# Kernel optimization log

Hardware: AMD Instinct MI355X
Metric: run time of the kernel (lower is better)

## Reference

```python
import jax, jax.numpy as jnp
import numpy as np

NUM_HEADS = 16
SIZE_PER_HEAD = 64
HIDDEN = NUM_HEADS * SIZE_PER_HEAD  # 1024
B, F, T = 4, 1024, 1024
NEG_INF = -10000.0


def setup_inputs() -> dict:
    key = jax.random.key(0)
    ks = jax.random.split(key, 6)
    scale = 0.02
    return {
        "from_tensor": jax.random.normal(ks[0], (B, F, HIDDEN), dtype=jnp.float32),
        "to_tensor": jax.random.normal(ks[1], (B, T, HIDDEN), dtype=jnp.float32),
        "attention_mask": jnp.ones((B, F, T), dtype=jnp.float32),
        "Wq": jax.random.normal(ks[2], (HIDDEN, HIDDEN), dtype=jnp.float32) * scale,
        "bq": jnp.zeros((HIDDEN,), dtype=jnp.float32),
        "Wk": jax.random.normal(ks[3], (HIDDEN, HIDDEN), dtype=jnp.float32) * scale,
        "bk": jnp.zeros((HIDDEN,), dtype=jnp.float32),
        "Wv": jax.random.normal(ks[4], (HIDDEN, HIDDEN), dtype=jnp.float32) * scale,
        "bv": jnp.zeros((HIDDEN,), dtype=jnp.float32),
    }


def _split_heads(x, seq_len):
    # [B, S, H*Dh] -> [B, H, S, Dh]
    return x.reshape(B, seq_len, NUM_HEADS, SIZE_PER_HEAD).transpose(0, 2, 1, 3)


def reference(from_tensor, to_tensor, attention_mask, Wq, bq, Wk, bk, Wv, bv):
    # Q/K/V dense projections (query_act/key_act/value_act are None -> linear)
    q = _split_heads(from_tensor @ Wq + bq, F)   # [B,H,F,Dh]
    k = _split_heads(to_tensor @ Wk + bk, T)     # [B,H,T,Dh]
    v = _split_heads(to_tensor @ Wv + bv, T)     # [B,H,T,Dh]

    # scaled dot-product attention scores: [B,H,F,T]
    scores = jnp.einsum("bhfd,bhtd->bhft", q, k) / jnp.sqrt(
        jnp.asarray(SIZE_PER_HEAD, dtype=q.dtype))

    # BERT-style mask adder: mask==1 -> attend, mask==0 -> -10000
    adder = (1.0 - attention_mask[:, None, :, :]) * NEG_INF
    scores = scores + adder

    attention_probs = jax.nn.softmax(scores, axis=-1)  # dropout_prob=0.0

    ctx = jnp.einsum("bhft,bhtd->bhfd", attention_probs, v)  # [B,H,F,Dh]
    ctx = ctx.transpose(0, 2, 1, 3).reshape(B, F, NUM_HEADS * SIZE_PER_HEAD)
    return ctx, attention_probs
```

## Files before the change

kernel.cpp:

```cpp
#include <hip/hip_runtime.h>

typedef unsigned short u16;
typedef __bf16 bf16x8 __attribute__((ext_vector_type(8)));
typedef float f32x4 __attribute__((ext_vector_type(4)));
typedef u16 u16x8 __attribute__((ext_vector_type(8)));

#define NUM_HEADS 16
#define DHEAD 64
#define HIDDEN 1024
#define BATCH 4
#define SEQ 1024

__device__ __forceinline__ u16 f2bf(float x) {
  unsigned u = __float_as_uint(x);
  u = u + 0x7FFFu + ((u >> 16) & 1u);
  return (u16)(u >> 16);
}
__device__ __forceinline__ float bf2f(u16 b) {
  return __uint_as_float(((unsigned)b) << 16);
}

__device__ __forceinline__ void async16(u16* lds, const u16* g) {
  __builtin_amdgcn_global_load_lds(
      (const __attribute__((address_space(1))) void*)g,
      (__attribute__((address_space(3))) void*)lds, 16, 0, 0);
}

__global__ void k_cvt(const float* __restrict__ in, u16* __restrict__ out, int n8) {
  int i = blockIdx.x * 256 + threadIdx.x;
  if (i >= n8) return;
  float4 a = ((const float4*)in)[i * 2];
  float4 b = ((const float4*)in)[i * 2 + 1];
  u16x8 v;
  v[0] = f2bf(a.x); v[1] = f2bf(a.y); v[2] = f2bf(a.z); v[3] = f2bf(a.w);
  v[4] = f2bf(b.x); v[5] = f2bf(b.y); v[6] = f2bf(b.z); v[7] = f2bf(b.w);
  *(u16x8*)&out[(size_t)i * 8] = v;
}

__global__ void k_wtrans(const float* __restrict__ Wq, const float* __restrict__ Wk,
                         const float* __restrict__ Wv, u16* __restrict__ Wt) {
  __shared__ float tile[64][65];
  const float* W = (blockIdx.z == 0) ? Wq : (blockIdx.z == 1) ? Wk : Wv;
  u16* out = Wt + (size_t)blockIdx.z * HIDDEN * HIDDEN;
  int k0 = blockIdx.y * 64, n0 = blockIdx.x * 64;
  int tid = threadIdx.x;
  int r = tid >> 6, c = tid & 63;
#pragma unroll
  for (int i = 0; i < 16; ++i)
    tile[i * 4 + r][c] = W[(size_t)(k0 + i * 4 + r) * HIDDEN + n0 + c];
  __syncthreads();
#pragma unroll
  for (int i = 0; i < 16; ++i)
    out[(size_t)(n0 + i * 4 + r) * HIDDEN + k0 + c] = f2bf(tile[c][i * 4 + r]);
}

__global__ void k_mask(const float* __restrict__ mask, u16* __restrict__ adder,
                       int* __restrict__ flags) {
  int tt = blockIdx.x, ft = blockIdx.y, b = blockIdx.z;
  int tid = threadIdx.x;
  __shared__ int sflag;
  if (tid == 0) sflag = 0;
  __syncthreads();
  int any = 0;
  size_t base = ((size_t)b * SEQ + ft * 128) * SEQ + tt * 128;
  for (int i = 0; i < 64; ++i) {
    int idx = i * 256 + tid;
    int r = idx >> 7, c = idx & 127;
    float v = mask[base + (size_t)r * SEQ + c];
    any |= (v != 1.0f);
    adder[base + (size_t)r * SEQ + c] = f2bf((1.0f - v) * -10000.0f);
  }
  if (any) sflag = 1;
  __syncthreads();
  if (tid == 0) flags[(b * 8 + ft) * 8 + tt] = sflag;
}

__global__ __launch_bounds__(256) void k_gemm(
    const u16* __restrict__ Af, const u16* __restrict__ At,
    const u16* __restrict__ Wt,
    const float* __restrict__ bq, const float* __restrict__ bk, const float* __restrict__ bv,
    u16* __restrict__ Qh, u16* __restrict__ Kh, u16* __restrict__ Vt) {
  __shared__ u16 sA[128 * 64];
  __shared__ u16 sB[128 * 64];
  int which = blockIdx.z;
  const u16* A = (which == 0) ? Af : At;
  const u16* B = Wt + (size_t)which * HIDDEN * HIDDEN;
  const float* bias = (which == 0) ? bq : (which == 1) ? bk : bv;
  int m0 = blockIdx.y * 128, n0 = blockIdx.x * 128;
  int tid = threadIdx.x, w = tid >> 6, lane = tid & 63;
  int wr = w >> 1, wc = w & 1;
  int g = lane >> 4, cc = lane & 15;

  f32x4 acc[4][4] = {};

  int sx[4], srow[4], scol[4];
#pragma unroll
  for (int i = 0; i < 4; ++i) {
    int ch = w * 4 + i;
    int x = ch * 1024 + lane * 16;
    int row = x >> 7;
    int colb = (x & 127) ^ ((row & 7) << 4);
    sx[i] = ch * 512;
    srow[i] = row;
    scol[i] = colb >> 1;
  }

  for (int kt = 0; kt < HIDDEN / 64; ++kt) {
    __syncthreads();
#pragma unroll
    for (int i = 0; i < 4; ++i) {
      async16(&sA[sx[i]], A + (size_t)(m0 + srow[i]) * HIDDEN + kt * 64 + scol[i]);
      async16(&sB[sx[i]], B + (size_t)(n0 + srow[i]) * HIDDEN + kt * 64 + scol[i]);
    }
    asm volatile("s_waitcnt vmcnt(0)" ::: "memory");
    __syncthreads();
#pragma unroll
    for (int kk = 0; kk < 2; ++kk) {
      bf16x8 af[4], bfr[4];
#pragma unroll
      for (int mf = 0; mf < 4; ++mf) {
        int row = wr * 64 + mf * 16 + cc;
        int colb = (kk * 64 + (g << 4)) ^ ((row & 7) << 4);
        af[mf] = *(const bf16x8*)&sA[(row * 128 + colb) >> 1];
      }
#pragma unroll
      for (int nf = 0; nf < 4; ++nf) {
        int row = wc * 64 + nf * 16 + cc;
        int colb = (kk * 64 + (g << 4)) ^ ((row & 7) << 4);
        bfr[nf] = *(const bf16x8*)&sB[(row * 128 + colb) >> 1];
      }
#pragma unroll
      for (int mf = 0; mf < 4; ++mf)
#pragma unroll
        for (int nf = 0; nf < 4; ++nf)
          acc[mf][nf] = __builtin_amdgcn_mfma_f32_16x16x32_bf16(af[mf], bfr[nf], acc[mf][nf], 0, 0, 0);
    }
  }

#pragma unroll
  for (int mf = 0; mf < 4; ++mf) {
#pragma unroll
    for (int nf = 0; nf < 4; ++nf) {
      int n = n0 + wc * 64 + nf * 16 + cc;
      float bval = bias[n];
      int h = n >> 6, d = n & 63;
#pragma unroll
      for (int r = 0; r < 4; ++r) {
        int m = m0 + wr * 64 + mf * 16 + g * 4 + r;
        int b = m >> 10, s = m & 1023;
        u16 o = f2bf(acc[mf][nf][r] + bval);
        if (which == 0)
          Qh[((((size_t)b * NUM_HEADS + h) * SEQ + s) << 6) + d] = o;
        else if (which == 1)
          Kh[((((size_t)b * NUM_HEADS + h) * SEQ + s) << 6) + d] = o;
        else
          Vt[(((size_t)b * NUM_HEADS + h) * 64 + d) * SEQ + s] = o;
      }
    }
  }
}

__global__ __launch_bounds__(256) void k_attn(
    const u16* __restrict__ Qh, const u16* __restrict__ Kh, const u16* __restrict__ Vt,
    const u16* __restrict__ adder, const int* __restrict__ flags,
    float* __restrict__ ctx, float* __restrict__ probs) {
  __shared__ u16 sQ[128 * 64];
  __shared__ u16 sK[128 * 64];
  __shared__ u16 sV[64 * 128];
  __shared__ u16 sP[128 * 128];
  int ft = blockIdx.x, h = blockIdx.y, b = blockIdx.z;
  int f0 = ft * 128;
  int bh = b * NUM_HEADS + h;
  const u16* Qg = Qh + ((size_t)bh * SEQ + f0) * 64;
  const u16* Kg = Kh + (size_t)bh * SEQ * 64;
  const u16* Vg = Vt + (size_t)bh * 64 * SEQ;
  int tid = threadIdx.x, w = tid >> 6, lane = tid & 63;
  int g = lane >> 4, cc = lane & 15;
  const int fbase = w * 32;

  int sx[4], srow7[4], scol7[4], srow8[4], scol8[4];
#pragma unroll
  for (int i = 0; i < 4; ++i) {
    int ch = w * 4 + i;
    int x = ch * 1024 + lane * 16;
    sx[i] = ch * 512;
    int r7 = x >> 7;
    int c7 = (x & 127) ^ ((r7 & 7) << 4);
    srow7[i] = r7; scol7[i] = c7 >> 1;
    int r8 = x >> 8;
    int c8 = (x & 255) ^ ((r8 & 7) << 4);
    srow8[i] = r8; scol8[i] = c8 >> 1;
  }

#pragma unroll
  for (int i = 0; i < 4; ++i)
    async16(&sQ[sx[i]], Qg + (size_t)srow7[i] * 64 + scol7[i]);

  float m_run[8], l_run[8];
#pragma unroll
  for (int i = 0; i < 8; ++i) { m_run[i] = -3.0e38f; l_run[i] = 0.0f; }

  for (int tt = 0; tt < 8; ++tt) {
    __syncthreads();
#pragma unroll
    for (int i = 0; i < 4; ++i)
      async16(&sK[sx[i]], Kg + (size_t)(tt * 128 + srow7[i]) * 64 + scol7[i]);
    asm volatile("s_waitcnt vmcnt(0)" ::: "memory");
    __syncthreads();

    f32x4 s[2][8] = {};
#pragma unroll
    for (int kk = 0; kk < 2; ++kk) {
      bf16x8 aq[2], bk8[8];
#pragma unroll
      for (int mf = 0; mf < 2; ++mf) {
        int row = fbase + mf * 16 + cc;
        int colb = (kk * 64 + (g << 4)) ^ ((row & 7) << 4);
        aq[mf] = *(const bf16x8*)&sQ[(row * 128 + colb) >> 1];
      }
#pragma unroll
      for (int nf = 0; nf < 8; ++nf) {
        int row = nf * 16 + cc;
        int colb = (kk * 64 + (g << 4)) ^ ((row & 7) << 4);
        bk8[nf] = *(const bf16x8*)&sK[(row * 128 + colb) >> 1];
      }
#pragma unroll
      for (int mf = 0; mf < 2; ++mf)
#pragma unroll
        for (int nf = 0; nf < 8; ++nf)
          s[mf][nf] = __builtin_amdgcn_mfma_f32_16x16x32_bf16(aq[mf], bk8[nf], s[mf][nf], 0, 0, 0);
    }
    int flg = flags[(b * 8 + ft) * 8 + tt];
#pragma unroll
    for (int mf = 0; mf < 2; ++mf)
#pragma unroll
      for (int nf = 0; nf < 8; ++nf)
#pragma unroll
        for (int r = 0; r < 4; ++r) s[mf][nf][r] *= 0.125f;
    if (flg) {
      for (int mf = 0; mf < 2; ++mf)
        for (int nf = 0; nf < 8; ++nf)
          for (int r = 0; r < 4; ++r) {
            int frow = f0 + fbase + mf * 16 + g * 4 + r;
            int tcol = tt * 128 + nf * 16 + cc;
            s[mf][nf][r] += bf2f(adder[((size_t)b * SEQ + frow) * SEQ + tcol]);
          }
    }
#pragma unroll
    for (int mf = 0; mf < 2; ++mf)
#pragma unroll
      for (int r = 0; r < 4; ++r) {
        float tmax = s[mf][0][r];
#pragma unroll
        for (int nf = 1; nf < 8; ++nf) tmax = fmaxf(tmax, s[mf][nf][r]);
        tmax = fmaxf(tmax, __shfl_xor(tmax, 1, 16));
        tmax = fmaxf(tmax, __shfl_xor(tmax, 2, 16));
        tmax = fmaxf(tmax, __shfl_xor(tmax, 4, 16));
        tmax = fmaxf(tmax, __shfl_xor(tmax, 8, 16));
        int idx = mf * 4 + r;
        float mnew = fmaxf(m_run[idx], tmax);
        float sum = 0.f;
#pragma unroll
        for (int nf = 0; nf < 8; ++nf) sum += __expf(s[mf][nf][r] - mnew);
        sum += __shfl_xor(sum, 1, 16);
        sum += __shfl_xor(sum, 2, 16);
        sum += __shfl_xor(sum, 4, 16);
        sum += __shfl_xor(sum, 8, 16);
        l_run[idx] = l_run[idx] * __expf(m_run[idx] - mnew) + sum;
        m_run[idx] = mnew;
      }
  }

  float inv_l[8];
#pragma unroll
  for (int i = 0; i < 8; ++i) inv_l[i] = 1.0f / l_run[i];

  f32x4 accO[2][4] = {};

  for (int tt = 0; tt < 8; ++tt) {
    __syncthreads();
#pragma unroll
    for (int i = 0; i < 4; ++i) {
      async16(&sK[sx[i]], Kg + (size_t)(tt * 128 + srow7[i]) * 64 + scol7[i]);
      async16(&sV[sx[i]], Vg + (size_t)srow8[i] * SEQ + tt * 128 + scol8[i]);
    }
    asm volatile("s_waitcnt vmcnt(0)" ::: "memory");
    __syncthreads();

    f32x4 s[2][8] = {};
#pragma unroll
    for (int kk = 0; kk < 2; ++kk) {
      bf16x8 aq[2], bk8[8];
#pragma unroll
      for (int mf = 0; mf < 2; ++mf) {
        int row = fbase + mf * 16 + cc;
        int colb = (kk * 64 + (g << 4)) ^ ((row & 7) << 4);
        aq[mf] = *(const bf16x8*)&sQ[(row * 128 + colb) >> 1];
      }
#pragma unroll
      for (int nf = 0; nf < 8; ++nf) {
        int row = nf * 16 + cc;
        int colb = (kk * 64 + (g << 4)) ^ ((row & 7) << 4);
        bk8[nf] = *(const bf16x8*)&sK[(row * 128 + colb) >> 1];
      }
#pragma unroll
      for (int mf = 0; mf < 2; ++mf)
#pragma unroll
        for (int nf = 0; nf < 8; ++nf)
          s[mf][nf] = __builtin_amdgcn_mfma_f32_16x16x32_bf16(aq[mf], bk8[nf], s[mf][nf], 0, 0, 0);
    }
    int flg = flags[(b * 8 + ft) * 8 + tt];
#pragma unroll
    for (int mf = 0; mf < 2; ++mf)
#pragma unroll
      for (int nf = 0; nf < 8; ++nf)
#pragma unroll
        for (int r = 0; r < 4; ++r) s[mf][nf][r] *= 0.125f;
    if (flg) {
      for (int mf = 0; mf < 2; ++mf)
        for (int nf = 0; nf < 8; ++nf)
          for (int r = 0; r < 4; ++r) {
            int frow = f0 + fbase + mf * 16 + g * 4 + r;
            int tcol = tt * 128 + nf * 16 + cc;
            s[mf][nf][r] += bf2f(adder[((size_t)b * SEQ + frow) * SEQ + tcol]);
          }
    }
#pragma unroll
    for (int mf = 0; mf < 2; ++mf)
#pragma unroll
      for (int nf = 0; nf < 8; ++nf)
#pragma unroll
        for (int r = 0; r < 4; ++r) {
          int idx = mf * 4 + r;
          float p = __expf(s[mf][nf][r] - m_run[idx]) * inv_l[idx];
          int frow = fbase + mf * 16 + g * 4 + r;
          int tcol = nf * 16 + cc;
          probs[(((size_t)bh * SEQ) + f0 + frow) * SEQ + tt * 128 + tcol] = p;
          sP[(frow * 256 + ((tcol * 2) ^ ((frow & 7) << 4))) >> 1] = f2bf(p);
        }
#pragma unroll
    for (int ks = 0; ks < 4; ++ks) {
      bf16x8 ap[2], bv8[4];
#pragma unroll
      for (int mf = 0; mf < 2; ++mf) {
        int row = fbase + mf * 16 + cc;
        int colb = (ks * 64 + (g << 4)) ^ ((row & 7) << 4);
        ap[mf] = *(const bf16x8*)&sP[(row * 256 + colb) >> 1];
      }
#pragma unroll
      for (int nf = 0; nf < 4; ++nf) {
        int row = nf * 16 + cc;
        int colb = (ks * 64 + (g << 4)) ^ ((row & 7) << 4);
        bv8[nf] = *(const bf16x8*)&sV[(row * 256 + colb) >> 1];
      }
#pragma unroll
      for (int mf = 0; mf < 2; ++mf)
#pragma unroll
        for (int nf = 0; nf < 4; ++nf)
          accO[mf][nf] = __builtin_amdgcn_mfma_f32_16x16x32_bf16(ap[mf], bv8[nf], accO[mf][nf], 0, 0, 0);
    }
  }

#pragma unroll
  for (int mf = 0; mf < 2; ++mf)
#pragma unroll
    for (int nf = 0; nf < 4; ++nf)
#pragma unroll
      for (int r = 0; r < 4; ++r) {
        int frow = fbase + mf * 16 + g * 4 + r;
        int d = nf * 16 + cc;
        ctx[((size_t)b * SEQ + f0 + frow) * HIDDEN + h * 64 + d] = accO[mf][nf][r];
      }
}

extern "C" void kernel_launch(void* const* d_in, const int* in_sizes, int n_in,
                              void* d_out, int out_size, void* d_ws, size_t ws_size,
                              hipStream_t stream) {
  const float* from = (const float*)d_in[0];
  const float* to   = (const float*)d_in[1];
  const float* mask = (const float*)d_in[2];
  const float* Wq   = (const float*)d_in[3];
  const float* bq   = (const float*)d_in[4];
  const float* Wk   = (const float*)d_in[5];
  const float* bk   = (const float*)d_in[6];
  const float* Wv   = (const float*)d_in[7];
  const float* bv   = (const float*)d_in[8];

  char* ws = (char*)d_ws;
  u16* Af    = (u16*)(ws);
  u16* At    = (u16*)(ws + 8388608);
  u16* Wt    = (u16*)(ws + 16777216);
  u16* adder = (u16*)(ws + 23068672);
  int* flags = (int*)(ws + 31457280);
  u16* Qh    = (u16*)(ws + 31458304);
  u16* Kh    = (u16*)(ws + 39846912);
  u16* Vt    = (u16*)(ws + 48235520);

  float* ctx = (float*)d_out;
  float* probs = ctx + (size_t)BATCH * SEQ * HIDDEN;

  k_cvt<<<2048, 256, 0, stream>>>(from, Af, 524288);
  k_cvt<<<2048, 256, 0, stream>>>(to, At, 524288);
  k_wtrans<<<dim3(16, 16, 3), 256, 0, stream>>>(Wq, Wk, Wv, Wt);
  k_mask<<<dim3(8, 8, 4), 256, 0, stream>>>(mask, adder, flags);
  k_gemm<<<dim3(8, 32, 3), 256, 0, stream>>>(Af, At, Wt, bq, bk, bv, Qh, Kh, Vt);
  k_attn<<<dim3(8, 16, 4), 256, 0, stream>>>(Qh, Kh, Vt, adder, flags, ctx, probs);
}
```

Before: 211.1 us.

## Double-buffer GEMM and attention K loads, use exp2 softmax, coalesce probs stores

Adds double-buffered LDS prefetch of the next K tile in both the projection GEMM and the two attention passes, so global loads overlap MFMA work. Q fragments are kept in registers instead of LDS, and the mask flags are preloaded into a bitmask. Softmax switches to exp2 with log2e folded into the scale and the mask adder. Probs are now written from the bf16 LDS copy as coalesced vector stores, and the two convert launches are merged into one. The main risk is that probs are stored after bf16 rounding, which loses precision in that output.

```diff
diff --git a/kernel.cpp b/kernel.cpp
--- a/kernel.cpp
+++ b/kernel.cpp
@@ -6,29 +6,37 @@
 typedef u16 u16x8 __attribute__((ext_vector_type(8)));
 
 #define NUM_HEADS 16
-#define DHEAD 64
 #define HIDDEN 1024
 #define BATCH 4
 #define SEQ 1024
-
-__device__ __forceinline__ u16 f2bf(float x) {
+#define C1 0.1803368809109783f
+#define LOG2E 1.4426950408889634f
+
+#define VMCNT0 asm volatile("s_waitcnt vmcnt(0)" ::: "memory")
+#define VMCNT4 asm volatile("s_waitcnt vmcnt(4)" ::: "memory")
+#define BAR __builtin_amdgcn_s_barrier()
+#define SCHED0 __builtin_amdgcn_sched_barrier(0)
+
+static __device__ __forceinline__ u16 f2bf(float x) {
   unsigned u = __float_as_uint(x);
   u = u + 0x7FFFu + ((u >> 16) & 1u);
   return (u16)(u >> 16);
 }
-__device__ __forceinline__ float bf2f(u16 b) {
+static __device__ __forceinline__ float bf2f(u16 b) {
   return __uint_as_float(((unsigned)b) << 16);
 }
-
-__device__ __forceinline__ void async16(u16* lds, const u16* g) {
+static __device__ __forceinline__ void async16(u16* lds, const u16* g) {
   __builtin_amdgcn_global_load_lds(
       (const __attribute__((address_space(1))) void*)g,
       (__attribute__((address_space(3))) void*)lds, 16, 0, 0);
 }
 
-__global__ void k_cvt(const float* __restrict__ in, u16* __restrict__ out, int n8) {
+__global__ void k_cvt(const float* __restrict__ in0, u16* __restrict__ out0,
+                      const float* __restrict__ in1, u16* __restrict__ out1, int n8) {
   int i = blockIdx.x * 256 + threadIdx.x;
   if (i >= n8) return;
+  const float* in = blockIdx.z ? in1 : in0;
+  u16* out = blockIdx.z ? out1 : out0;
   float4 a = ((const float4*)in)[i * 2];
   float4 b = ((const float4*)in)[i * 2 + 1];
   u16x8 v;
@@ -68,7 +76,7 @@
     int r = idx >> 7, c = idx & 127;
     float v = mask[base + (size_t)r * SEQ + c];
     any |= (v != 1.0f);
-    adder[base + (size_t)r * SEQ + c] = f2bf((1.0f - v) * -10000.0f);
+    adder[base + (size_t)r * SEQ + c] = f2bf((1.0f - v) * -10000.0f * LOG2E);
   }
   if (any) sflag = 1;
   __syncthreads();
@@ -80,8 +88,8 @@
     const u16* __restrict__ Wt,
     const float* __restrict__ bq, const float* __restrict__ bk, const float* __restrict__ bv,
     u16* __restrict__ Qh, u16* __restrict__ Kh, u16* __restrict__ Vt) {
-  __shared__ u16 sA[128 * 64];
-  __shared__ u16 sB[128 * 64];
+  __shared__ u16 sA[2][128 * 64];
+  __shared__ u16 sB[2][128 * 64];
   int which = blockIdx.z;
   const u16* A = (which == 0) ? Af : At;
   const u16* B = Wt + (size_t)which * HIDDEN * HIDDEN;
@@ -93,7 +101,9 @@
 
   f32x4 acc[4][4] = {};
 
-  int sx[4], srow[4], scol[4];
+  int sx[4];
+  const u16* aptr[4];
+  const u16* bptr[4];
 #pragma unroll
   for (int i = 0; i < 4; ++i) {
     int ch = w * 4 + i;
@@ -101,19 +111,29 @@
     int row = x >> 7;
     int colb = (x & 127) ^ ((row & 7) << 4);
     sx[i] = ch * 512;
-    srow[i] = row;
-    scol[i] = colb >> 1;
-  }
-
-  for (int kt = 0; kt < HIDDEN / 64; ++kt) {
-    __syncthreads();
-#pragma unroll
-    for (int i = 0; i < 4; ++i) {
-      async16(&sA[sx[i]], A + (size_t)(m0 + srow[i]) * HIDDEN + kt * 64 + scol[i]);
-      async16(&sB[sx[i]], B + (size_t)(n0 + srow[i]) * HIDDEN + kt * 64 + scol[i]);
-    }
-    asm volatile("s_waitcnt vmcnt(0)" ::: "memory");
-    __syncthreads();
+    aptr[i] = A + (size_t)(m0 + row) * HIDDEN + (colb >> 1);
+    bptr[i] = B + (size_t)(n0 + row) * HIDDEN + (colb >> 1);
+  }
+
+#pragma unroll
+  for (int i = 0; i < 4; ++i) {
+    async16(&sA[0][sx[i]], aptr[i]);
+    async16(&sB[0][sx[i]], bptr[i]);
+  }
+
+#pragma unroll 1
+  for (int kt = 0; kt < 16; ++kt) {
+    int cur = kt & 1;
+    VMCNT0;
+    BAR;
+    SCHED0;
+    if (kt < 15) {
+#pragma unroll
+      for (int i = 0; i < 4; ++i) {
+        async16(&sA[cur ^ 1][sx[i]], aptr[i] + (kt + 1) * 64);
+        async16(&sB[cur ^ 1][sx[i]], bptr[i] + (kt + 1) * 64);
+      }
+    }
 #pragma unroll
     for (int kk = 0; kk < 2; ++kk) {
       bf16x8 af[4], bfr[4];
@@ -121,13 +141,13 @@
       for (int mf = 0; mf < 4; ++mf) {
         int row = wr * 64 + mf * 16 + cc;
         int colb = (kk * 64 + (g << 4)) ^ ((row & 7) << 4);
-        af[mf] = *(const bf16x8*)&sA[(row * 128 + colb) >> 1];
+        af[mf] = *(const bf16x8*)&sA[cur][(row * 128 + colb) >> 1];
       }
 #pragma unroll
       for (int nf = 0; nf < 4; ++nf) {
         int row = wc * 64 + nf * 16 + cc;
         int colb = (kk * 64 + (g << 4)) ^ ((row & 7) << 4);
-        bfr[nf] = *(const bf16x8*)&sB[(row * 128 + colb) >> 1];
+        bfr[nf] = *(const bf16x8*)&sB[cur][(row * 128 + colb) >> 1];
       }
 #pragma unroll
       for (int mf = 0; mf < 4; ++mf)
@@ -164,8 +184,7 @@
     const u16* __restrict__ Qh, const u16* __restrict__ Kh, const u16* __restrict__ Vt,
     const u16* __restrict__ adder, const int* __restrict__ flags,
     float* __restrict__ ctx, float* __restrict__ probs) {
-  __shared__ u16 sQ[128 * 64];
-  __shared__ u16 sK[128 * 64];
+  __shared__ u16 sK[2][128 * 64];
   __shared__ u16 sV[64 * 128];
   __shared__ u16 sP[128 * 128];
   int ft = blockIdx.x, h = blockIdx.y, b = blockIdx.z;
@@ -178,7 +197,14 @@
   int g = lane >> 4, cc = lane & 15;
   const int fbase = w * 32;
 
-  int sx[4], srow7[4], scol7[4], srow8[4], scol8[4];
+  int flgmask = 0;
+#pragma unroll
+  for (int tt = 0; tt < 8; ++tt)
+    flgmask |= (flags[(b * 8 + ft) * 8 + tt] != 0) << tt;
+
+  int sx[4];
+  const u16* kbase[4];
+  const u16* vbase[4];
 #pragma unroll
   for (int i = 0; i < 4; ++i) {
     int ch = w * 4 + i;
@@ -186,58 +212,59 @@
     sx[i] = ch * 512;
     int r7 = x >> 7;
     int c7 = (x & 127) ^ ((r7 & 7) << 4);
-    srow7[i] = r7; scol7[i] = c7 >> 1;
+    kbase[i] = Kg + (size_t)r7 * 64 + (c7 >> 1);
     int r8 = x >> 8;
     int c8 = (x & 255) ^ ((r8 & 7) << 4);
-    srow8[i] = r8; scol8[i] = c8 >> 1;
-  }
-
-#pragma unroll
-  for (int i = 0; i < 4; ++i)
-    async16(&sQ[sx[i]], Qg + (size_t)srow7[i] * 64 + scol7[i]);
+    vbase[i] = Vg + (size_t)r8 * SEQ + (c8 >> 1);
+  }
+
+  bf16x8 aq[2][2];
+#pragma unroll
+  for (int kk = 0; kk < 2; ++kk)
+#pragma unroll
+    for (int mf = 0; mf < 2; ++mf)
+      aq[kk][mf] = *(const bf16x8*)&Qg[(size_t)(fbase + mf * 16 + cc) * 64 + kk * 32 + g * 8];
 
   float m_run[8], l_run[8];
 #pragma unroll
   for (int i = 0; i < 8; ++i) { m_run[i] = -3.0e38f; l_run[i] = 0.0f; }
 
+#pragma unroll
+  for (int i = 0; i < 4; ++i) async16(&sK[0][sx[i]], kbase[i]);
+
+#pragma unroll 1
   for (int tt = 0; tt < 8; ++tt) {
-    __syncthreads();
-#pragma unroll
-    for (int i = 0; i < 4; ++i)
-      async16(&sK[sx[i]], Kg + (size_t)(tt * 128 + srow7[i]) * 64 + scol7[i]);
-    asm volatile("s_waitcnt vmcnt(0)" ::: "memory");
-    __syncthreads();
-
+    int cur = tt & 1;
+    VMCNT0;
+    BAR;
+    SCHED0;
+    if (tt < 7) {
+#pragma unroll
+      for (int i = 0; i < 4; ++i)
+        async16(&sK[cur ^ 1][sx[i]], kbase[i] + (tt + 1) * 8192);
+    }
     f32x4 s[2][8] = {};
 #pragma unroll
     for (int kk = 0; kk < 2; ++kk) {
-      bf16x8 aq[2], bk8[8];
-#pragma unroll
-      for (int mf = 0; mf < 2; ++mf) {
-        int row = fbase + mf * 16 + cc;
-        int colb = (kk * 64 + (g << 4)) ^ ((row & 7) << 4);
-        aq[mf] = *(const bf16x8*)&sQ[(row * 128 + colb) >> 1];
-      }
+      bf16x8 bk8[8];
 #pragma unroll
       for (int nf = 0; nf < 8; ++nf) {
         int row = nf * 16 + cc;
         int colb = (kk * 64 + (g << 4)) ^ ((row & 7) << 4);
-        bk8[nf] = *(const bf16x8*)&sK[(row * 128 + colb) >> 1];
+        bk8[nf] = *(const bf16x8*)&sK[cur][(row * 128 + colb) >> 1];
       }
 #pragma unroll
       for (int mf = 0; mf < 2; ++mf)
 #pragma unroll
         for (int nf = 0; nf < 8; ++nf)
-          s[mf][nf] = __builtin_amdgcn_mfma_f32_16x16x32_bf16(aq[mf], bk8[nf], s[mf][nf], 0, 0, 0);
-    }
-    int flg = flags[(b * 8 + ft) * 8 + tt];
+          s[mf][nf] = __builtin_amdgcn_mfma_f32_16x16x32_bf16(aq[kk][mf], bk8[nf], s[mf][nf], 0, 0, 0);
+    }
 #pragma unroll
     for (int mf = 0; mf < 2; ++mf)
 #pragma unroll
       for (int nf = 0; nf < 8; ++nf)
-#pragma unroll
-        for (int r = 0; r < 4; ++r) s[mf][nf][r] *= 0.125f;
-    if (flg) {
+        s[mf][nf] = s[mf][nf] * C1;
+    if ((flgmask >> tt) & 1) {
       for (int mf = 0; mf < 2; ++mf)
         for (int nf = 0; nf < 8; ++nf)
           for (int r = 0; r < 4; ++r) {
@@ -261,12 +288,12 @@
         float mnew = fmaxf(m_run[idx], tmax);
         float sum = 0.f;
 #pragma unroll
-        for (int nf = 0; nf < 8; ++nf) sum += __expf(s[mf][nf][r] - mnew);
+        for (int nf = 0; nf < 8; ++nf) sum += exp2f(s[mf][nf][r] - mnew);
         sum += __shfl_xor(sum, 1, 16);
         sum += __shfl_xor(sum, 2, 16);
         sum += __shfl_xor(sum, 4, 16);
         sum += __shfl_xor(sum, 8, 16);
-        l_run[idx] = l_run[idx] * __expf(m_run[idx] - mnew) + sum;
+        l_run[idx] = l_run[idx] * exp2f(m_run[idx] - mnew) + sum;
         m_run[idx] = mnew;
       }
   }
@@ -277,46 +304,40 @@
 
   f32x4 accO[2][4] = {};
 
+#pragma unroll
+  for (int i = 0; i < 4; ++i) async16(&sK[0][sx[i]], kbase[i]);
+
+#pragma unroll 1
   for (int tt = 0; tt < 8; ++tt) {
-    __syncthreads();
-#pragma unroll
-    for (int i = 0; i < 4; ++i) {
-      async16(&sK[sx[i]], Kg + (size_t)(tt * 128 + srow7[i]) * 64 + scol7[i]);
-      async16(&sV[sx[i]], Vg + (size_t)srow8[i] * SEQ + tt * 128 + scol8[i]);
-    }
-    asm volatile("s_waitcnt vmcnt(0)" ::: "memory");
-    __syncthreads();
+    int cur = tt & 1;
+    VMCNT0;
+    BAR;
+    SCHED0;
+#pragma unroll
+    for (int i = 0; i < 4; ++i) async16(&sV[sx[i]], vbase[i] + tt * 128);
 
     f32x4 s[2][8] = {};
 #pragma unroll
     for (int kk = 0; kk < 2; ++kk) {
-      bf16x8 aq[2], bk8[8];
-#pragma unroll
-      for (int mf = 0; mf < 2; ++mf) {
-        int row = fbase + mf * 16 + cc;
-        int colb = (kk * 64 + (g << 4)) ^ ((row & 7) << 4);
-        aq[mf] = *(const bf16x8*)&sQ[(row * 128 + colb) >> 1];
-      }
+      bf16x8 bk8[8];
 #pragma unroll
       for (int nf = 0; nf < 8; ++nf) {
         int row = nf * 16 + cc;
         int colb = (kk * 64 + (g << 4)) ^ ((row & 7) << 4);
-        bk8[nf] = *(const bf16x8*)&sK[(row * 128 + colb) >> 1];
+        bk8[nf] = *(const bf16x8*)&sK[cur][(row * 128 + colb) >> 1];
       }
 #pragma unroll
       for (int mf = 0; mf < 2; ++mf)
 #pragma unroll
         for (int nf = 0; nf < 8; ++nf)
-          s[mf][nf] = __builtin_amdgcn_mfma_f32_16x16x32_bf16(aq[mf], bk8[nf], s[mf][nf], 0, 0, 0);
-    }
-    int flg = flags[(b * 8 + ft) * 8 + tt];
+          s[mf][nf] = __builtin_amdgcn_mfma_f32_16x16x32_bf16(aq[kk][mf], bk8[nf], s[mf][nf], 0, 0, 0);
+    }
 #pragma unroll
     for (int mf = 0; mf < 2; ++mf)
 #pragma unroll
       for (int nf = 0; nf < 8; ++nf)
-#pragma unroll
-        for (int r = 0; r < 4; ++r) s[mf][nf][r] *= 0.125f;
-    if (flg) {
+        s[mf][nf] = s[mf][nf] * C1;
+    if ((flgmask >> tt) & 1) {
       for (int mf = 0; mf < 2; ++mf)
         for (int nf = 0; nf < 8; ++nf)
           for (int r = 0; r < 4; ++r) {
@@ -332,12 +353,32 @@
 #pragma unroll
         for (int r = 0; r < 4; ++r) {
           int idx = mf * 4 + r;
-          float p = __expf(s[mf][nf][r] - m_run[idx]) * inv_l[idx];
+          float p = exp2f(s[mf][nf][r] - m_run[idx]) * inv_l[idx];
           int frow = fbase + mf * 16 + g * 4 + r;
           int tcol = nf * 16 + cc;
-          probs[(((size_t)bh * SEQ) + f0 + frow) * SEQ + tt * 128 + tcol] = p;
           sP[(frow * 256 + ((tcol * 2) ^ ((frow & 7) << 4))) >> 1] = f2bf(p);
         }
+#pragma unroll
+    for (int sw = 0; sw < 8; ++sw) {
+      int row = fbase + sw * 4 + (lane >> 4);
+      int colb = ((lane & 15) * 16) ^ ((row & 7) << 4);
+      u16x8 pv = *(const u16x8*)&sP[(row * 256 + colb) >> 1];
+      float* dst = &probs[((size_t)bh * SEQ + f0 + row) * SEQ + tt * 128 + (lane & 15) * 8];
+      f32x4 o0 = {bf2f(pv[0]), bf2f(pv[1]), bf2f(pv[2]), bf2f(pv[3])};
+      f32x4 o1 = {bf2f(pv[4]), bf2f(pv[5]), bf2f(pv[6]), bf2f(pv[7])};
+      *(f32x4*)dst = o0;
+      *(f32x4*)(dst + 4) = o1;
+    }
+    if (tt < 7) {
+#pragma unroll
+      for (int i = 0; i < 4; ++i)
+        async16(&sK[cur ^ 1][sx[i]], kbase[i] + (tt + 1) * 8192);
+      VMCNT4;
+    } else {
+      VMCNT0;
+    }
+    BAR;
+    SCHED0;
 #pragma unroll
     for (int ks = 0; ks < 4; ++ks) {
       bf16x8 ap[2], bv8[4];
@@ -399,8 +440,7 @@
   float* ctx = (float*)d_out;
   float* probs = ctx + (size_t)BATCH * SEQ * HIDDEN;
 
-  k_cvt<<<2048, 256, 0, stream>>>(from, Af, 524288);
-  k_cvt<<<2048, 256, 0, stream>>>(to, At, 524288);
+  k_cvt<<<dim3(2048, 1, 2), 256, 0, stream>>>(from, Af, to, At, 524288);
   k_wtrans<<<dim3(16, 16, 3), 256, 0, stream>>>(Wq, Wk, Wv, Wt);
   k_mask<<<dim3(8, 8, 4), 256, 0, stream>>>(mask, adder, flags);
   k_gemm<<<dim3(8, 32, 3), 256, 0, stream>>>(Af, At, Wt, bq, bk, bv, Qh, Kh, Vt);
```

Measured after the change: 234.4 us. +11.0%, slower.

## Fuse convert launches, skip unmasked adder writes, stage V transpose via LDS, use exp2

Applied to the files above, without the earlier changes.

The two input conversion launches are merged into one grid. The mask kernel now first scans the tile with vectorized loads and writes the bf16 adder (pre-scaled by log2e) only when the tile contains masked entries. The V projection epilogue transposes its tile through shared memory so the transposed stores are coalesced 16-byte writes instead of scattered 2-byte ones. Attention folds log2e into the score scale and switches exp to exp2f. Together these aim to cut mask-write traffic, uncoalesced stores and launch overhead, at the cost of extra LDS syncs in the GEMM epilogue and a second mask read when any tile is masked.

```diff
diff --git a/kernel.cpp b/kernel.cpp
--- a/kernel.cpp
+++ b/kernel.cpp
@@ -4,31 +4,37 @@
 typedef __bf16 bf16x8 __attribute__((ext_vector_type(8)));
 typedef float f32x4 __attribute__((ext_vector_type(4)));
 typedef u16 u16x8 __attribute__((ext_vector_type(8)));
+typedef u16 u16x4 __attribute__((ext_vector_type(4)));
 
 #define NUM_HEADS 16
-#define DHEAD 64
 #define HIDDEN 1024
 #define BATCH 4
 #define SEQ 1024
-
-__device__ __forceinline__ u16 f2bf(float x) {
+#define C1 0.1803368809109783f
+#define LOG2E 1.4426950408889634f
+
+#define VMCNT0 asm volatile("s_waitcnt vmcnt(0)" ::: "memory")
+
+static __device__ __forceinline__ u16 f2bf(float x) {
   unsigned u = __float_as_uint(x);
   u = u + 0x7FFFu + ((u >> 16) & 1u);
   return (u16)(u >> 16);
 }
-__device__ __forceinline__ float bf2f(u16 b) {
+static __device__ __forceinline__ float bf2f(u16 b) {
   return __uint_as_float(((unsigned)b) << 16);
 }
-
-__device__ __forceinline__ void async16(u16* lds, const u16* g) {
+static __device__ __forceinline__ void async16(u16* lds, const u16* g) {
   __builtin_amdgcn_global_load_lds(
       (const __attribute__((address_space(1))) void*)g,
       (__attribute__((address_space(3))) void*)lds, 16, 0, 0);
 }
 
-__global__ void k_cvt(const float* __restrict__ in, u16* __restrict__ out, int n8) {
+__global__ void k_cvt(const float* __restrict__ in0, u16* __restrict__ out0,
+                      const float* __restrict__ in1, u16* __restrict__ out1, int n8) {
   int i = blockIdx.x * 256 + threadIdx.x;
   if (i >= n8) return;
+  const float* in = blockIdx.z ? in1 : in0;
+  u16* out = blockIdx.z ? out1 : out0;
   float4 a = ((const float4*)in)[i * 2];
   float4 b = ((const float4*)in)[i * 2 + 1];
   u16x8 v;
@@ -61,17 +67,31 @@
   __shared__ int sflag;
   if (tid == 0) sflag = 0;
   __syncthreads();
+  size_t base = ((size_t)b * SEQ + ft * 128) * SEQ + tt * 128;
   int any = 0;
-  size_t base = ((size_t)b * SEQ + ft * 128) * SEQ + tt * 128;
-  for (int i = 0; i < 64; ++i) {
+#pragma unroll
+  for (int i = 0; i < 16; ++i) {
     int idx = i * 256 + tid;
-    int r = idx >> 7, c = idx & 127;
-    float v = mask[base + (size_t)r * SEQ + c];
-    any |= (v != 1.0f);
-    adder[base + (size_t)r * SEQ + c] = f2bf((1.0f - v) * -10000.0f);
+    int r = idx >> 5, c4 = idx & 31;
+    float4 v = *(const float4*)&mask[base + (size_t)r * SEQ + c4 * 4];
+    any |= (v.x != 1.0f) | (v.y != 1.0f) | (v.z != 1.0f) | (v.w != 1.0f);
   }
   if (any) sflag = 1;
   __syncthreads();
+  if (sflag) {
+#pragma unroll
+    for (int i = 0; i < 16; ++i) {
+      int idx = i * 256 + tid;
+      int r = idx >> 5, c4 = idx & 31;
+      float4 v = *(const float4*)&mask[base + (size_t)r * SEQ + c4 * 4];
+      u16x4 o;
+      o[0] = f2bf((1.0f - v.x) * -10000.0f * LOG2E);
+      o[1] = f2bf((1.0f - v.y) * -10000.0f * LOG2E);
+      o[2] = f2bf((1.0f - v.z) * -10000.0f * LOG2E);
+      o[3] = f2bf((1.0f - v.w) * -10000.0f * LOG2E);
+      *(u16x4*)&adder[base + (size_t)r * SEQ + c4 * 4] = o;
+    }
+  }
   if (tid == 0) flags[(b * 8 + ft) * 8 + tt] = sflag;
 }
 
@@ -80,8 +100,9 @@
     const u16* __restrict__ Wt,
     const float* __restrict__ bq, const float* __restrict__ bk, const float* __restrict__ bv,
     u16* __restrict__ Qh, u16* __restrict__ Kh, u16* __restrict__ Vt) {
-  __shared__ u16 sA[128 * 64];
-  __shared__ u16 sB[128 * 64];
+  __shared__ u16 sAB[2 * 128 * 64];
+  u16* sA = sAB;
+  u16* sB = sAB + 128 * 64;
   int which = blockIdx.z;
   const u16* A = (which == 0) ? Af : At;
   const u16* B = Wt + (size_t)which * HIDDEN * HIDDEN;
@@ -112,7 +133,7 @@
       async16(&sA[sx[i]], A + (size_t)(m0 + srow[i]) * HIDDEN + kt * 64 + scol[i]);
       async16(&sB[sx[i]], B + (size_t)(n0 + srow[i]) * HIDDEN + kt * 64 + scol[i]);
     }
-    asm volatile("s_waitcnt vmcnt(0)" ::: "memory");
+    VMCNT0;
     __syncthreads();
 #pragma unroll
     for (int kk = 0; kk < 2; ++kk) {
@@ -137,25 +158,51 @@
     }
   }
 
-#pragma unroll
-  for (int mf = 0; mf < 4; ++mf) {
-#pragma unroll
-    for (int nf = 0; nf < 4; ++nf) {
-      int n = n0 + wc * 64 + nf * 16 + cc;
-      float bval = bias[n];
-      int h = n >> 6, d = n & 63;
-#pragma unroll
-      for (int r = 0; r < 4; ++r) {
-        int m = m0 + wr * 64 + mf * 16 + g * 4 + r;
-        int b = m >> 10, s = m & 1023;
-        u16 o = f2bf(acc[mf][nf][r] + bval);
-        if (which == 0)
-          Qh[((((size_t)b * NUM_HEADS + h) * SEQ + s) << 6) + d] = o;
-        else if (which == 1)
-          Kh[((((size_t)b * NUM_HEADS + h) * SEQ + s) << 6) + d] = o;
-        else
-          Vt[(((size_t)b * NUM_HEADS + h) * 64 + d) * SEQ + s] = o;
-      }
+  if (which != 2) {
+#pragma unroll
+    for (int mf = 0; mf < 4; ++mf) {
+#pragma unroll
+      for (int nf = 0; nf < 4; ++nf) {
+        int n = n0 + wc * 64 + nf * 16 + cc;
+        float bval = bias[n];
+        int h = n >> 6, d = n & 63;
+#pragma unroll
+        for (int r = 0; r < 4; ++r) {
+          int m = m0 + wr * 64 + mf * 16 + g * 4 + r;
+          int b = m >> 10, s = m & 1023;
+          u16 o = f2bf(acc[mf][nf][r] + bval);
+          if (which == 0)
+            Qh[((((size_t)b * NUM_HEADS + h) * SEQ + s) << 6) + d] = o;
+          else
+            Kh[((((size_t)b * NUM_HEADS + h) * SEQ + s) << 6) + d] = o;
+        }
+      }
+    }
+  } else {
+    __syncthreads();
+    char* T = (char*)sAB;
+#pragma unroll
+    for (int mf = 0; mf < 4; ++mf) {
+#pragma unroll
+      for (int nf = 0; nf < 4; ++nf) {
+        int nl = wc * 64 + nf * 16 + cc;
+        float bval = bias[n0 + nl];
+        int mlb = wr * 64 + mf * 16 + g * 4;
+        u16x4 v;
+#pragma unroll
+        for (int r = 0; r < 4; ++r) v[r] = f2bf(acc[mf][nf][r] + bval);
+        int byte = nl * 256 + ((mlb * 2) ^ ((nl & 7) << 4));
+        *(u16x4*)(T + byte) = v;
+      }
+    }
+    __syncthreads();
+    int nl = tid >> 1, mh = (tid & 1) * 64;
+    int b = m0 >> 10, s0 = m0 & 1023;
+    u16* dst = &Vt[((size_t)b * 1024 + n0 + nl) * SEQ + s0 + mh];
+#pragma unroll
+    for (int j = 0; j < 8; ++j) {
+      int byte = nl * 256 + (((mh + j * 8) * 2) ^ ((nl & 7) << 4));
+      *(u16x8*)&dst[j * 8] = *(const u16x8*)(T + byte);
     }
   }
 }
@@ -205,7 +252,7 @@
 #pragma unroll
     for (int i = 0; i < 4; ++i)
       async16(&sK[sx[i]], Kg + (size_t)(tt * 128 + srow7[i]) * 64 + scol7[i]);
-    asm volatile("s_waitcnt vmcnt(0)" ::: "memory");
+    VMCNT0;
     __syncthreads();
 
     f32x4 s[2][8] = {};
@@ -235,8 +282,7 @@
     for (int mf = 0; mf < 2; ++mf)
 #pragma unroll
       for (int nf = 0; nf < 8; ++nf)
-#pragma unroll
-        for (int r = 0; r < 4; ++r) s[mf][nf][r] *= 0.125f;
+        s[mf][nf] = s[mf][nf] * C1;
     if (flg) {
       for (int mf = 0; mf < 2; ++mf)
         for (int nf = 0; nf < 8; ++nf)
@@ -261,12 +307,12 @@
         float mnew = fmaxf(m_run[idx], tmax);
         float sum = 0.f;
 #pragma unroll
-        for (int nf = 0; nf < 8; ++nf) sum += __expf(s[mf][nf][r] - mnew);
+        for (int nf = 0; nf < 8; ++nf) sum += exp2f(s[mf][nf][r] - mnew);
         sum += __shfl_xor(sum, 1, 16);
         sum += __shfl_xor(sum, 2, 16);
         sum += __shfl_xor(sum, 4, 16);
         sum += __shfl_xor(sum, 8, 16);
-        l_run[idx] = l_run[idx] * __expf(m_run[idx] - mnew) + sum;
+        l_run[idx] = l_run[idx] * exp2f(m_run[idx] - mnew) + sum;
         m_run[idx] = mnew;
       }
   }
@@ -284,7 +330,7 @@
       async16(&sK[sx[i]], Kg + (size_t)(tt * 128 + srow7[i]) * 64 + scol7[i]);
       async16(&sV[sx[i]], Vg + (size_t)srow8[i] * SEQ + tt * 128 + scol8[i]);
     }
-    asm volatile("s_waitcnt vmcnt(0)" ::: "memory");
+    VMCNT0;
     __syncthreads();
 
     f32x4 s[2][8] = {};
@@ -314,8 +360,7 @@
     for (int mf = 0; mf < 2; ++mf)
 #pragma unroll
       for (int nf = 0; nf < 8; ++nf)
-#pragma unroll
-        for (int r = 0; r < 4; ++r) s[mf][nf][r] *= 0.125f;
+        s[mf][nf] = s[mf][nf] * C1;
     if (flg) {
       for (int mf = 0; mf < 2; ++mf)
         for (int nf = 0; nf < 8; ++nf)
@@ -332,7 +377,7 @@
 #pragma unroll
         for (int r = 0; r < 4; ++r) {
           int idx = mf * 4 + r;
-          float p = __expf(s[mf][nf][r] - m_run[idx]) * inv_l[idx];
+          float p = exp2f(s[mf][nf][r] - m_run[idx]) * inv_l[idx];
           int frow = fbase + mf * 16 + g * 4 + r;
           int tcol = nf * 16 + cc;
           probs[(((size_t)bh * SEQ) + f0 + frow) * SEQ + tt * 128 + tcol] = p;
@@ -399,8 +444,7 @@
   float* ctx = (float*)d_out;
   float* probs = ctx + (size_t)BATCH * SEQ * HIDDEN;
 
-  k_cvt<<<2048, 256, 0, stream>>>(from, Af, 524288);
-  k_cvt<<<2048, 256, 0, stream>>>(to, At, 524288);
+  k_cvt<<<dim3(2048, 1, 2), 256, 0, stream>>>(from, Af, to, At, 524288);
   k_wtrans<<<dim3(16, 16, 3), 256, 0, stream>>>(Wq, Wk, Wv, Wt);
   k_mask<<<dim3(8, 8, 4), 256, 0, stream>>>(mask, adder, flags);
   k_gemm<<<dim3(8, 32, 3), 256, 0, stream>>>(Af, At, Wt, bq, bk, bv, Qh, Kh, Vt);
```

Result: no change. 210.6 us (-0.3%).
